# Performance work log

Hardware: AMD Instinct MI355X
Metric: run time of the kernel (lower is better)

The kernel has to match this reference:

```python
import jax, jax.numpy as jnp
import numpy as np

S, X, G = 2048, 2048, 2
INPUT_SIZE = (3, 32, 32)
F = int(np.prod(INPUT_SIZE))


def setup_inputs() -> dict:
    key = jax.random.key(0)
    k1, k2, k3 = jax.random.split(key, 3)
    samples = jax.random.normal(k1, (S,) + INPUT_SIZE, dtype=jnp.float32)
    x = jax.random.normal(k2, (X,) + INPUT_SIZE, dtype=jnp.float32)
    # per-feature std per gradation, kept in [0.1, 1.0) like ranges_std scaling
    std = jax.random.uniform(k3, (G, F), dtype=jnp.float32, minval=0.1, maxval=1.0)
    return {"samples": samples, "x": x, "std": std}


def reference(samples, x, std):
    # samples: [S, C, H, W], x: [X, C, H, W], std: [G, F]
    G_, F_ = std.shape
    s = samples.reshape(samples.shape[0], F_)  # [S, F]
    xf = x.reshape(x.shape[0], F_)             # [X, F]
    w = 1.0 / (std * std)                       # [G, F] precision
    # per-gradation normalizer: -0.5*F*log(2pi) - sum_f log(std)
    const = -0.5 * F_ * jnp.log(2.0 * jnp.pi) - jnp.sum(jnp.log(std), axis=1)  # [G]
    # sum_f -0.5*((s-x)/std)^2 expanded: -0.5*(s^2 w - 2 s w x + x^2 w)
    A = jnp.einsum('sf,gf->gs', s * s, w)        # [G, S]
    C = jnp.einsum('xf,gf->gx', xf * xf, w)      # [G, X]
    B = jnp.einsum('sf,gf,xf->gsx', s, w, xf)    # [G, S, X] cross term
    logits = -0.5 * (A[:, :, None] - 2.0 * B + C[:, None, :]) + const[:, None, None]
    lp = jax.nn.logsumexp(logits, axis=2)        # over x (mixture components)
    lp = jax.nn.logsumexp(lp, axis=0)            # over gradations
    return lp - jnp.log(jnp.float32(x.shape[0] * G_))
```

## Files before the change

### kernel.cpp

```cpp
#include <hip/hip_runtime.h>
#include <math.h>
#include <stdint.h>

#define S_N 2048
#define X_N 2048
#define G_N 2
#define F_N 3072

#define TM 256
#define TN 128
#define BK 64
#define ITERS (F_N / BK)
#define NBUF 3

typedef __bf16 bf16;
typedef __bf16 bf16x4 __attribute__((ext_vector_type(4)));
typedef __bf16 bf16x8 __attribute__((ext_vector_type(8)));
typedef float f32x4 __attribute__((ext_vector_type(4)));
typedef int i32x4 __attribute__((ext_vector_type(4)));

__device__ __forceinline__ void gload_lds16(const bf16* g, void* l) {
  __builtin_amdgcn_global_load_lds(
      (const __attribute__((address_space(1))) void*)g,
      (__attribute__((address_space(3))) void*)l, 16, 0, 0);
}

__global__ void k_const(const float* __restrict__ stdv, float* __restrict__ constg,
                        float* __restrict__ rinv) {
  int g = blockIdx.x;
  int t = threadIdx.x;
  float s = 0.f;
  for (int f = t; f < F_N; f += 256) {
    float v = stdv[g * F_N + f];
    rinv[g * F_N + f] = 1.0f / v;
    s += logf(v);
  }
  for (int o = 32; o; o >>= 1) s += __shfl_xor(s, o);
  __shared__ float red[4];
  int w = t >> 6, l = t & 63;
  if (l == 0) red[w] = s;
  __syncthreads();
  if (t == 0) {
    float tot = red[0] + red[1] + red[2] + red[3];
    constg[g] = -0.5f * (float)F_N * 1.8378770664093453f - tot;
  }
}

__global__ void k_prep(const float* __restrict__ samples, const float* __restrict__ xin,
                       const float* __restrict__ rinv,
                       bf16* __restrict__ U, bf16* __restrict__ V,
                       float* __restrict__ A, float* __restrict__ C) {
  int r = blockIdx.x;
  int t = threadIdx.x;
  bool isS = (r < S_N);
  const float* src = isS ? (samples + (size_t)r * F_N) : (xin + (size_t)(r - S_N) * F_N);
  float4 row[3];
#pragma unroll
  for (int j = 0; j < 3; ++j) row[j] = ((const float4*)src)[t + j * 256];

  __shared__ float red[4];
  int w = t >> 6, l = t & 63;

  for (int g = 0; g < G_N; ++g) {
    const float4* sd = (const float4*)(rinv + (size_t)g * F_N);
    bf16* dst = isS ? (U + ((size_t)g * S_N + r) * F_N)
                    : (V + ((size_t)g * X_N + (r - S_N)) * F_N);
    float acc = 0.f;
#pragma unroll
    for (int j = 0; j < 3; ++j) {
      float4 d = sd[t + j * 256];
      float u0 = row[j].x * d.x;
      float u1 = row[j].y * d.y;
      float u2 = row[j].z * d.z;
      float u3 = row[j].w * d.w;
      bf16x4 b;
      b[0] = (bf16)u0; b[1] = (bf16)u1; b[2] = (bf16)u2; b[3] = (bf16)u3;
      float f0 = (float)b[0], f1 = (float)b[1], f2 = (float)b[2], f3 = (float)b[3];
      acc += f0 * f0 + f1 * f1 + f2 * f2 + f3 * f3;
      ((bf16x4*)dst)[t + j * 256] = b;
    }
    for (int o = 32; o; o >>= 1) acc += __shfl_xor(acc, o);
    __syncthreads();
    if (l == 0) red[w] = acc;
    __syncthreads();
    if (t == 0) {
      float tot = red[0] + red[1] + red[2] + red[3];
      if (isS) A[(size_t)g * S_N + r] = tot;
      else     C[(size_t)g * X_N + (r - S_N)] = tot;
    }
  }
}

__global__ __launch_bounds__(512, 2) void k_gemm(const bf16* __restrict__ U, const bf16* __restrict__ V,
                                                 const float* __restrict__ A, const float* __restrict__ C,
                                                 float* __restrict__ logits) {
  __shared__ i32x4 ldsA[NBUF][TM * BK / 8];
  __shared__ i32x4 ldsB[NBUF][TN * BK / 8];

  int t = threadIdx.x;
  int g = blockIdx.z;
  int bm = blockIdx.y * TM;
  int bn = blockIdx.x * TN;

  const bf16* Ub = U + ((size_t)g * S_N + bm) * F_N;
  const bf16* Vb = V + ((size_t)g * X_N + bn) * F_N;

  int wave = t >> 6, lane = t & 63;
  int wm = wave & 3, wn = wave >> 2;
  int r = lane & 15, q = lane >> 4;
  int fr = (r >> 1) & 7;
  int ck0 = q ^ fr;
  int ck1 = (4 | q) ^ fr;
  int abase = (wm * 64 + r) * 8;
  int bbase = (wn * 64 + r) * 8;

  int row0 = t >> 3;
  int gcc = (t & 7) ^ ((t >> 4) & 7);
  const bf16* gA[4];
  const bf16* gB[2];
#pragma unroll
  for (int j = 0; j < 4; ++j) gA[j] = Ub + (size_t)(row0 + j * 64) * F_N + gcc * 8;
#pragma unroll
  for (int j = 0; j < 2; ++j) gB[j] = Vb + (size_t)(row0 + j * 64) * F_N + gcc * 8;

  f32x4 acc[4][4] = {};

#pragma unroll
  for (int j = 0; j < 4; ++j) gload_lds16(gA[j], &ldsA[0][t + j * 512]);
#pragma unroll
  for (int j = 0; j < 2; ++j) gload_lds16(gB[j], &ldsB[0][t + j * 512]);
#pragma unroll
  for (int j = 0; j < 4; ++j) gload_lds16(gA[j] + BK, &ldsA[1][t + j * 512]);
#pragma unroll
  for (int j = 0; j < 2; ++j) gload_lds16(gB[j] + BK, &ldsB[1][t + j * 512]);
  asm volatile("s_waitcnt vmcnt(6)" ::: "memory");
  __builtin_amdgcn_s_barrier();

  int cur = 0;
  for (int it = 0; it < ITERS; ++it) {
    int k2 = it + 2;
    int pk = (k2 < ITERS ? k2 : 0) * BK;
    int stg = (cur >= 1) ? cur - 1 : 2;
    const i32x4* LA = ldsA[cur];
    const i32x4* LB = ldsB[cur];

    gload_lds16(gA[0] + pk, &ldsA[stg][t]);
    gload_lds16(gA[1] + pk, &ldsA[stg][t + 512]);
    gload_lds16(gA[2] + pk, &ldsA[stg][t + 1024]);
    bf16x8 af[4][2], b01[2][2];
#pragma unroll
    for (int mi = 0; mi < 4; ++mi) {
      af[mi][0] = __builtin_bit_cast(bf16x8, LA[abase + mi * 128 + ck0]);
      af[mi][1] = __builtin_bit_cast(bf16x8, LA[abase + mi * 128 + ck1]);
    }
#pragma unroll
    for (int ni = 0; ni < 2; ++ni) {
      b01[ni][0] = __builtin_bit_cast(bf16x8, LB[bbase + ni * 128 + ck0]);
      b01[ni][1] = __builtin_bit_cast(bf16x8, LB[bbase + ni * 128 + ck1]);
    }
    __builtin_amdgcn_s_barrier();
    asm volatile("s_waitcnt lgkmcnt(0)" ::: "memory");
    __builtin_amdgcn_sched_barrier(0);
    __builtin_amdgcn_s_setprio(1);
#pragma unroll
    for (int ks = 0; ks < 2; ++ks)
#pragma unroll
      for (int mi = 0; mi < 4; ++mi)
#pragma unroll
        for (int ni = 0; ni < 2; ++ni)
          acc[mi][ni] = __builtin_amdgcn_mfma_f32_16x16x32_bf16(af[mi][ks], b01[ni][ks], acc[mi][ni], 0, 0, 0);
    __builtin_amdgcn_s_setprio(0);
    __builtin_amdgcn_s_barrier();

    gload_lds16(gA[3] + pk, &ldsA[stg][t + 1536]);
    gload_lds16(gB[0] + pk, &ldsB[stg][t]);
    gload_lds16(gB[1] + pk, &ldsB[stg][t + 512]);
    bf16x8 b23[2][2];
#pragma unroll
    for (int ni = 0; ni < 2; ++ni) {
      b23[ni][0] = __builtin_bit_cast(bf16x8, LB[bbase + (2 + ni) * 128 + ck0]);
      b23[ni][1] = __builtin_bit_cast(bf16x8, LB[bbase + (2 + ni) * 128 + ck1]);
    }
    asm volatile("s_waitcnt vmcnt(6)" ::: "memory");
    __builtin_amdgcn_s_barrier();
    asm volatile("s_waitcnt lgkmcnt(0)" ::: "memory");
    __builtin_amdgcn_sched_barrier(0);
    __builtin_amdgcn_s_setprio(1);
#pragma unroll
    for (int ks = 0; ks < 2; ++ks)
#pragma unroll
      for (int mi = 0; mi < 4; ++mi)
#pragma unroll
        for (int ni = 0; ni < 2; ++ni)
          acc[mi][2 + ni] = __builtin_amdgcn_mfma_f32_16x16x32_bf16(af[mi][ks], b23[ni][ks], acc[mi][2 + ni], 0, 0, 0);
    __builtin_amdgcn_s_setprio(0);
    __builtin_amdgcn_s_barrier();

    cur = (cur == 2) ? 0 : cur + 1;
  }

  const float* Ap = A + (size_t)g * S_N + bm + wm * 64;
  const float* Cp = C + (size_t)g * X_N + bn + wn * 64;
  float cv[4];
#pragma unroll
  for (int ni = 0; ni < 4; ++ni) cv[ni] = Cp[ni * 16 + r];
#pragma unroll
  for (int mi = 0; mi < 4; ++mi) {
#pragma unroll
    for (int i = 0; i < 4; ++i) {
      int rowl = wm * 64 + mi * 16 + q * 4 + i;
      float av = Ap[mi * 16 + q * 4 + i];
      float* orow = logits + ((size_t)g * S_N + bm + rowl) * X_N + bn + wn * 64;
#pragma unroll
      for (int ni = 0; ni < 4; ++ni)
        orow[ni * 16 + r] = acc[mi][ni][i] - 0.5f * (av + cv[ni]);
    }
  }
}

__global__ void k_lse(const float* __restrict__ logits, const float* __restrict__ constg,
                      float* __restrict__ out) {
  int s = blockIdx.x, t = threadIdx.x;
  float c0 = constg[0], c1 = constg[1];
  const float4* p0 = (const float4*)(logits + (size_t)s * X_N);
  const float4* p1 = (const float4*)(logits + ((size_t)S_N + s) * X_N);
  float4 v[4];
  v[0] = p0[t]; v[1] = p0[t + 256];
  v[2] = p1[t]; v[3] = p1[t + 256];
  v[0].x += c0; v[0].y += c0; v[0].z += c0; v[0].w += c0;
  v[1].x += c0; v[1].y += c0; v[1].z += c0; v[1].w += c0;
  v[2].x += c1; v[2].y += c1; v[2].z += c1; v[2].w += c1;
  v[3].x += c1; v[3].y += c1; v[3].z += c1; v[3].w += c1;

  float m = v[0].x;
#pragma unroll
  for (int j = 0; j < 4; ++j) {
    m = fmaxf(m, v[j].x); m = fmaxf(m, v[j].y);
    m = fmaxf(m, v[j].z); m = fmaxf(m, v[j].w);
  }
  for (int o = 32; o; o >>= 1) m = fmaxf(m, __shfl_xor(m, o));
  __shared__ float redm[4];
  __shared__ float reds[4];
  int w = t >> 6, l = t & 63;
  if (l == 0) redm[w] = m;
  __syncthreads();
  m = fmaxf(fmaxf(redm[0], redm[1]), fmaxf(redm[2], redm[3]));

  float sum = 0.f;
#pragma unroll
  for (int j = 0; j < 4; ++j) {
    sum += expf(v[j].x - m) + expf(v[j].y - m) + expf(v[j].z - m) + expf(v[j].w - m);
  }
  for (int o = 32; o; o >>= 1) sum += __shfl_xor(sum, o);
  if (l == 0) reds[w] = sum;
  __syncthreads();
  if (t == 0) {
    float tot = reds[0] + reds[1] + reds[2] + reds[3];
    out[s] = m + logf(tot) - 8.317766166719343f;
  }
}

extern "C" void kernel_launch(void* const* d_in, const int* in_sizes, int n_in,
                              void* d_out, int out_size, void* d_ws, size_t ws_size,
                              hipStream_t stream) {
  const float* samples = (const float*)d_in[0];
  const float* xin     = (const float*)d_in[1];
  const float* stdv    = (const float*)d_in[2];
  float* out = (float*)d_out;

  char* ws = (char*)d_ws;
  size_t off = 0;
  bf16* U = (bf16*)(ws + off);        off += (size_t)G_N * S_N * F_N * 2;
  bf16* V = (bf16*)(ws + off);        off += (size_t)G_N * X_N * F_N * 2;
  float* logits = (float*)(ws + off); off += (size_t)G_N * S_N * X_N * 4;
  float* A = (float*)(ws + off);      off += (size_t)G_N * S_N * 4;
  float* C = (float*)(ws + off);      off += (size_t)G_N * X_N * 4;
  float* constg = (float*)(ws + off); off += 256;
  float* rinv = (float*)(ws + off);   off += (size_t)G_N * F_N * 4;

  k_const<<<dim3(G_N), dim3(256), 0, stream>>>(stdv, constg, rinv);
  k_prep<<<dim3(S_N + X_N), dim3(256), 0, stream>>>(samples, xin, rinv, U, V, A, C);
  k_gemm<<<dim3(X_N / TN, S_N / TM, G_N), dim3(512), 0, stream>>>(U, V, A, C, logits);
  k_lse<<<dim3(S_N), dim3(256), 0, stream>>>(logits, constg, out);
}
```

Measured before the change: 189.9 us.

## Split K across wave pairs in GEMM and reduce partial tiles through LDS

```diff
diff --git a/kernel.cpp b/kernel.cpp
--- a/kernel.cpp
+++ b/kernel.cpp
@@ -94,8 +94,9 @@
 __global__ __launch_bounds__(512, 2) void k_gemm(const bf16* __restrict__ U, const bf16* __restrict__ V,
                                                  const float* __restrict__ A, const float* __restrict__ C,
                                                  float* __restrict__ logits) {
-  __shared__ i32x4 ldsA[NBUF][TM * BK / 8];
-  __shared__ i32x4 ldsB[NBUF][TN * BK / 8];
+  __shared__ i32x4 lds[NBUF * 2048 + NBUF * 1024];
+  i32x4* ldsA = lds;
+  i32x4* ldsB = lds + NBUF * 2048;
 
   int t = threadIdx.x;
   int g = blockIdx.z;
@@ -106,12 +107,14 @@
   const bf16* Vb = V + ((size_t)g * X_N + bn) * F_N;
 
   int wave = t >> 6, lane = t & 63;
-  int wm = wave & 3, wn = wave >> 2;
+  int pos = wave >> 1;
+  int kh = wave & 1;
+  int wm = pos >> 1;
+  int wn = pos & 1;
   int r = lane & 15, q = lane >> 4;
   int fr = (r >> 1) & 7;
-  int ck0 = q ^ fr;
-  int ck1 = (4 | q) ^ fr;
-  int abase = (wm * 64 + r) * 8;
+  int ck = (kh * 4 + q) ^ fr;
+  int abase = (wm * 128 + r) * 8;
   int bbase = (wn * 64 + r) * 8;
 
   int row0 = t >> 3;
@@ -123,16 +126,16 @@
 #pragma unroll
   for (int j = 0; j < 2; ++j) gB[j] = Vb + (size_t)(row0 + j * 64) * F_N + gcc * 8;
 
-  f32x4 acc[4][4] = {};
-
-#pragma unroll
-  for (int j = 0; j < 4; ++j) gload_lds16(gA[j], &ldsA[0][t + j * 512]);
-#pragma unroll
-  for (int j = 0; j < 2; ++j) gload_lds16(gB[j], &ldsB[0][t + j * 512]);
-#pragma unroll
-  for (int j = 0; j < 4; ++j) gload_lds16(gA[j] + BK, &ldsA[1][t + j * 512]);
-#pragma unroll
-  for (int j = 0; j < 2; ++j) gload_lds16(gB[j] + BK, &ldsB[1][t + j * 512]);
+  f32x4 acc[8][4] = {};
+
+#pragma unroll
+  for (int j = 0; j < 4; ++j) gload_lds16(gA[j], &ldsA[0 * 2048 + t + j * 512]);
+#pragma unroll
+  for (int j = 0; j < 2; ++j) gload_lds16(gB[j], &ldsB[0 * 1024 + t + j * 512]);
+#pragma unroll
+  for (int j = 0; j < 4; ++j) gload_lds16(gA[j] + BK, &ldsA[1 * 2048 + t + j * 512]);
+#pragma unroll
+  for (int j = 0; j < 2; ++j) gload_lds16(gB[j] + BK, &ldsB[1 * 1024 + t + j * 512]);
   asm volatile("s_waitcnt vmcnt(6)" ::: "memory");
   __builtin_amdgcn_s_barrier();
 
@@ -141,79 +144,111 @@
     int k2 = it + 2;
     int pk = (k2 < ITERS ? k2 : 0) * BK;
     int stg = (cur >= 1) ? cur - 1 : 2;
-    const i32x4* LA = ldsA[cur];
-    const i32x4* LB = ldsB[cur];
-
-    gload_lds16(gA[0] + pk, &ldsA[stg][t]);
-    gload_lds16(gA[1] + pk, &ldsA[stg][t + 512]);
-    gload_lds16(gA[2] + pk, &ldsA[stg][t + 1024]);
-    bf16x8 af[4][2], b01[2][2];
-#pragma unroll
-    for (int mi = 0; mi < 4; ++mi) {
-      af[mi][0] = __builtin_bit_cast(bf16x8, LA[abase + mi * 128 + ck0]);
-      af[mi][1] = __builtin_bit_cast(bf16x8, LA[abase + mi * 128 + ck1]);
-    }
-#pragma unroll
-    for (int ni = 0; ni < 2; ++ni) {
-      b01[ni][0] = __builtin_bit_cast(bf16x8, LB[bbase + ni * 128 + ck0]);
-      b01[ni][1] = __builtin_bit_cast(bf16x8, LB[bbase + ni * 128 + ck1]);
-    }
+    const i32x4* LA = ldsA + cur * 2048;
+    const i32x4* LB = ldsB + cur * 1024;
+
+    bf16x8 af[4], bfr[4];
+
+    gload_lds16(gA[0] + pk, &ldsA[stg * 2048 + t]);
+    gload_lds16(gA[1] + pk, &ldsA[stg * 2048 + t + 512]);
+    gload_lds16(gA[2] + pk, &ldsA[stg * 2048 + t + 1024]);
+#pragma unroll
+    for (int ni = 0; ni < 4; ++ni)
+      bfr[ni] = __builtin_bit_cast(bf16x8, LB[bbase + ni * 128 + ck]);
+#pragma unroll
+    for (int mi = 0; mi < 4; ++mi)
+      af[mi] = __builtin_bit_cast(bf16x8, LA[abase + mi * 128 + ck]);
     __builtin_amdgcn_s_barrier();
     asm volatile("s_waitcnt lgkmcnt(0)" ::: "memory");
     __builtin_amdgcn_sched_barrier(0);
     __builtin_amdgcn_s_setprio(1);
 #pragma unroll
-    for (int ks = 0; ks < 2; ++ks)
-#pragma unroll
-      for (int mi = 0; mi < 4; ++mi)
-#pragma unroll
-        for (int ni = 0; ni < 2; ++ni)
-          acc[mi][ni] = __builtin_amdgcn_mfma_f32_16x16x32_bf16(af[mi][ks], b01[ni][ks], acc[mi][ni], 0, 0, 0);
+    for (int mi = 0; mi < 4; ++mi)
+#pragma unroll
+      for (int ni = 0; ni < 4; ++ni)
+        acc[mi][ni] = __builtin_amdgcn_mfma_f32_16x16x32_bf16(af[mi], bfr[ni], acc[mi][ni], 0, 0, 0);
     __builtin_amdgcn_s_setprio(0);
     __builtin_amdgcn_s_barrier();
 
-    gload_lds16(gA[3] + pk, &ldsA[stg][t + 1536]);
-    gload_lds16(gB[0] + pk, &ldsB[stg][t]);
-    gload_lds16(gB[1] + pk, &ldsB[stg][t + 512]);
-    bf16x8 b23[2][2];
-#pragma unroll
-    for (int ni = 0; ni < 2; ++ni) {
-      b23[ni][0] = __builtin_bit_cast(bf16x8, LB[bbase + (2 + ni) * 128 + ck0]);
-      b23[ni][1] = __builtin_bit_cast(bf16x8, LB[bbase + (2 + ni) * 128 + ck1]);
-    }
+    gload_lds16(gA[3] + pk, &ldsA[stg * 2048 + t + 1536]);
+    gload_lds16(gB[0] + pk, &ldsB[stg * 1024 + t]);
+    gload_lds16(gB[1] + pk, &ldsB[stg * 1024 + t + 512]);
+#pragma unroll
+    for (int mi = 0; mi < 4; ++mi)
+      af[mi] = __builtin_bit_cast(bf16x8, LA[abase + (4 + mi) * 128 + ck]);
     asm volatile("s_waitcnt vmcnt(6)" ::: "memory");
     __builtin_amdgcn_s_barrier();
     asm volatile("s_waitcnt lgkmcnt(0)" ::: "memory");
     __builtin_amdgcn_sched_barrier(0);
     __builtin_amdgcn_s_setprio(1);
 #pragma unroll
-    for (int ks = 0; ks < 2; ++ks)
-#pragma unroll
-      for (int mi = 0; mi < 4; ++mi)
-#pragma unroll
-        for (int ni = 0; ni < 2; ++ni)
-          acc[mi][2 + ni] = __builtin_amdgcn_mfma_f32_16x16x32_bf16(af[mi][ks], b23[ni][ks], acc[mi][2 + ni], 0, 0, 0);
+    for (int mi = 0; mi < 4; ++mi)
+#pragma unroll
+      for (int ni = 0; ni < 4; ++ni)
+        acc[4 + mi][ni] = __builtin_amdgcn_mfma_f32_16x16x32_bf16(af[mi], bfr[ni], acc[4 + mi][ni], 0, 0, 0);
     __builtin_amdgcn_s_setprio(0);
     __builtin_amdgcn_s_barrier();
 
     cur = (cur == 2) ? 0 : cur + 1;
   }
 
-  const float* Ap = A + (size_t)g * S_N + bm + wm * 64;
-  const float* Cp = C + (size_t)g * X_N + bn + wn * 64;
-  float cv[4];
-#pragma unroll
-  for (int ni = 0; ni < 4; ++ni) cv[ni] = Cp[ni * 16 + r];
-#pragma unroll
-  for (int mi = 0; mi < 4; ++mi) {
+  asm volatile("s_waitcnt vmcnt(0)" ::: "memory");
+  __builtin_amdgcn_s_barrier();
+
+  f32x4* scr = (f32x4*)lds;
+  {
+    f32x4* mw = scr + wave * 1024;
+    if (kh == 0) {
+#pragma unroll
+      for (int mi = 0; mi < 8; ++mi)
+#pragma unroll
+        for (int nl = 0; nl < 2; ++nl)
+          mw[(mi * 2 + nl) * 64 + lane] = acc[mi][2 + nl];
+    } else {
+#pragma unroll
+      for (int mi = 0; mi < 8; ++mi)
+#pragma unroll
+        for (int nl = 0; nl < 2; ++nl)
+          mw[(mi * 2 + nl) * 64 + lane] = acc[mi][nl];
+    }
+  }
+  __syncthreads();
+  {
+    const f32x4* pw = scr + (wave ^ 1) * 1024;
+    if (kh == 0) {
+#pragma unroll
+      for (int mi = 0; mi < 8; ++mi)
+#pragma unroll
+        for (int nl = 0; nl < 2; ++nl)
+          acc[mi][nl] += pw[(mi * 2 + nl) * 64 + lane];
+    } else {
+#pragma unroll
+      for (int mi = 0; mi < 8; ++mi)
+#pragma unroll
+        for (int nl = 0; nl < 2; ++nl)
+          acc[mi][2 + nl] += pw[(mi * 2 + nl) * 64 + lane];
+    }
+  }
+
+  const float* Ap = A + (size_t)g * S_N + bm + wm * 128;
+  const float* Cp = C + (size_t)g * X_N + bn + wn * 64 + kh * 32;
+  float cv[2];
+#pragma unroll
+  for (int nl = 0; nl < 2; ++nl) cv[nl] = Cp[nl * 16 + r];
+#pragma unroll
+  for (int mi = 0; mi < 8; ++mi) {
 #pragma unroll
     for (int i = 0; i < 4; ++i) {
-      int rowl = wm * 64 + mi * 16 + q * 4 + i;
-      float av = Ap[mi * 16 + q * 4 + i];
-      float* orow = logits + ((size_t)g * S_N + bm + rowl) * X_N + bn + wn * 64;
-#pragma unroll
-      for (int ni = 0; ni < 4; ++ni)
-        orow[ni * 16 + r] = acc[mi][ni][i] - 0.5f * (av + cv[ni]);
+      int rowl = mi * 16 + q * 4 + i;
+      float av = Ap[rowl];
+      float* orow = logits + ((size_t)g * S_N + bm + wm * 128 + rowl) * X_N + bn + wn * 64 + kh * 32;
+      if (kh == 0) {
+        orow[r]      = acc[mi][0][i] - 0.5f * (av + cv[0]);
+        orow[16 + r] = acc[mi][1][i] - 0.5f * (av + cv[1]);
+      } else {
+        orow[r]      = acc[mi][2][i] - 0.5f * (av + cv[0]);
+        orow[16 + r] = acc[mi][3][i] - 0.5f * (av + cv[1]);
+      }
     }
   }
 }
```

Result: faster. 155.9 us (-17.9%).
